# Performance work log

Hardware: AMD Instinct MI355X
Metric: run time of the kernel (lower is better)

Reference implementation:

```python
import jax, jax.numpy as jnp
import numpy as np

EPS = 1e-08


def _similarity_transform(S1, S2):
    """Batched Procrustes: S1, S2 are [B, 3, N]. Returns aligned S1_hat [B, 3, N]."""
    mu1 = jnp.mean(S1, axis=-1, keepdims=True)          # [B,3,1]
    mu2 = jnp.mean(S2, axis=-1, keepdims=True)
    X1 = S1 - mu1
    X2 = S2 - mu2
    var1 = jnp.sum(X1 * X1, axis=(1, 2))                # [B]
    # cross-covariance K = X1 @ X2^T + eps (eps added to every entry, as in torch ref)
    K = jnp.einsum('bin,bjn->bij', X1, X2) + EPS        # [B,3,3]
    U, s, Vh = jnp.linalg.svd(K, full_matrices=False)
    V = jnp.swapaxes(Vh, -1, -2)
    # det(U @ V^T) = det(U @ Vh); sign has zero gradient, same as torch
    sign = jax.lax.stop_gradient(jnp.sign(jnp.linalg.det(jnp.matmul(U, Vh))))  # [B]
    ones = jnp.ones_like(sign)
    d = jnp.stack([ones, ones, sign], axis=-1)          # diag of Z, [B,3]
    # R = V @ Z @ U^T
    R = jnp.einsum('bik,bk,bjk->bij', V, d, U)          # [B,3,3]
    scale = jnp.einsum('bij,bji->b', R, K) / var1       # trace(R@K)/var1, [B]
    t = mu2 - scale[:, None, None] * jnp.matmul(R, mu1)  # [B,3,1]
    S1_hat = scale[:, None, None] * jnp.matmul(R, S1) + t
    return S1_hat


def setup_inputs() -> dict:
    key = jax.random.key(0)
    k1, k2 = jax.random.split(key)
    B, N = 1024, 6890
    pred = jax.random.normal(k1, (B, N, 3), dtype=jnp.float32)
    gt = jax.random.normal(k2, (B, N, 3), dtype=jnp.float32)
    return {"pred": pred, "gt": gt}


def reference(pred, gt):
    # inputs are [B, N, 3] -> torch code transposes to [B, 3, N] and back
    S1 = jnp.swapaxes(pred, 1, 2)
    S2 = jnp.swapaxes(gt, 1, 2)
    S1_hat = jnp.swapaxes(_similarity_transform(S1, S2), 1, 2)  # [B,N,3]
    # loss_type == 'l1', reduction='none'
    return jnp.abs(S1_hat - gt)
```

## Files before the change

kernel.cpp:

```cpp
#include <hip/hip_runtime.h>
#include <math.h>

#define NPTS 6890
#define BATCH 1024
#define FLOATS_PER_BATCH (NPTS * 3)
#define NGROUPS 1722
#define CHUNKS 4
#define GPC 431
#define HALF_GROUPS 861

__device__ __forceinline__ void accum(float* acc, float p0, float p1, float p2,
                                      float g0, float g1, float g2) {
  acc[0] += p0;  acc[1] += p1;  acc[2] += p2;
  acc[3] += g0;  acc[4] += g1;  acc[5] += g2;
  acc[6] += p0 * p0 + p1 * p1 + p2 * p2;
  acc[7]  += p0 * g0;  acc[8]  += p0 * g1;  acc[9]  += p0 * g2;
  acc[10] += p1 * g0;  acc[11] += p1 * g1;  acc[12] += p1 * g2;
  acc[13] += p2 * g0;  acc[14] += p2 * g1;  acc[15] += p2 * g2;
}

__device__ __forceinline__ void accum_grp(float* acc, const float4 a0,
                                          const float4 a1, const float4 a2,
                                          const float4 c0, const float4 c1,
                                          const float4 c2) {
  accum(acc, a0.x, a0.y, a0.z, c0.x, c0.y, c0.z);
  accum(acc, a0.w, a1.x, a1.y, c0.w, c1.x, c1.y);
  accum(acc, a1.z, a1.w, a2.x, c1.z, c1.w, c2.x);
  accum(acc, a2.y, a2.z, a2.w, c2.y, c2.z, c2.w);
}

__global__ __launch_bounds__(256) void reduce_kernel(
    const float* __restrict__ pred, const float* __restrict__ gt,
    float* __restrict__ partials) {
  const int b = blockIdx.y;
  const int c = blockIdx.x;
  const size_t ofs0 = (size_t)b * FLOATS_PER_BATCH;
  const int skip = (b & 1) ? 2 : 0;
  const size_t ofs = ofs0 + (size_t)skip * 3;
  const float4* __restrict__ p4 = (const float4*)(pred + ofs);
  const float4* __restrict__ g4 = (const float4*)(gt + ofs);

  const int start = c * GPC;
  const int end = (c == CHUNKS - 1) ? NGROUPS : (start + GPC);

  float acc[16];
#pragma unroll
  for (int i = 0; i < 16; ++i) acc[i] = 0.f;

  const int g0 = start + (int)threadIdx.x;
  const int g1 = g0 + 256;
  const bool has1 = (g1 < end);

  const float4 a0 = p4[3 * g0], a1 = p4[3 * g0 + 1], a2 = p4[3 * g0 + 2];
  const float4 c0 = g4[3 * g0], c1 = g4[3 * g0 + 1], c2 = g4[3 * g0 + 2];
  float4 b0, b1, b2, d0, d1, d2;
  if (has1) {
    b0 = p4[3 * g1]; b1 = p4[3 * g1 + 1]; b2 = p4[3 * g1 + 2];
    d0 = g4[3 * g1]; d1 = g4[3 * g1 + 1]; d2 = g4[3 * g1 + 2];
  }
  accum_grp(acc, a0, a1, a2, c0, c1, c2);
  if (has1) accum_grp(acc, b0, b1, b2, d0, d1, d2);

  if (c == 0 && threadIdx.x < 2) {
    const int n = skip ? (int)threadIdx.x : (NPTS - 2 + (int)threadIdx.x);
    const float* pp = pred + ofs0 + 3 * n;
    const float* gg = gt + ofs0 + 3 * n;
    accum(acc, pp[0], pp[1], pp[2], gg[0], gg[1], gg[2]);
  }

#pragma unroll
  for (int i = 0; i < 16; ++i) {
#pragma unroll
    for (int off = 32; off > 0; off >>= 1)
      acc[i] += __shfl_down(acc[i], off, 64);
  }

  __shared__ float red[4][16];
  const int wave = threadIdx.x >> 6;
  const int lane = threadIdx.x & 63;
  if (lane == 0) {
#pragma unroll
    for (int i = 0; i < 16; ++i) red[wave][i] = acc[i];
  }
  __syncthreads();
  if (threadIdx.x < 16) {
    const int i = threadIdx.x;
    partials[(b * CHUNKS + c) * 16 + i] =
        red[0][i] + red[1][i] + red[2][i] + red[3][i];
  }
}

__global__ void solve_kernel(const float* __restrict__ partials,
                             float* __restrict__ params) {
  const int b = blockIdx.x * blockDim.x + threadIdx.x;
  if (b >= BATCH) return;

  float s[16];
#pragma unroll
  for (int i = 0; i < 16; ++i) {
    s[i] = partials[(b * CHUNKS + 0) * 16 + i] +
           partials[(b * CHUNKS + 1) * 16 + i] +
           partials[(b * CHUNKS + 2) * 16 + i] +
           partials[(b * CHUNKS + 3) * 16 + i];
  }
  const double Ninv = 1.0 / (double)NPTS;

  double sp[3] = {s[0], s[1], s[2]};
  double sg[3] = {s[3], s[4], s[5]};
  double mu1[3], mu2[3];
#pragma unroll
  for (int i = 0; i < 3; ++i) { mu1[i] = sp[i] * Ninv; mu2[i] = sg[i] * Ninv; }
  const double var1 =
      (double)s[6] - (sp[0] * sp[0] + sp[1] * sp[1] + sp[2] * sp[2]) * Ninv;

  double K[3][3];
#pragma unroll
  for (int i = 0; i < 3; ++i)
#pragma unroll
    for (int j = 0; j < 3; ++j)
      K[i][j] = (double)s[7 + 3 * i + j] - sp[i] * sg[j] * Ninv + 1e-8;

  double A[3][3];
#pragma unroll
  for (int i = 0; i < 3; ++i)
#pragma unroll
    for (int j = 0; j < 3; ++j)
      A[i][j] = K[0][i] * K[0][j] + K[1][i] * K[1][j] + K[2][i] * K[2][j];

  double V[3][3] = {{1, 0, 0}, {0, 1, 0}, {0, 0, 1}};
  for (int sweep = 0; sweep < 10; ++sweep) {
    const double off = A[0][1] * A[0][1] + A[0][2] * A[0][2] + A[1][2] * A[1][2];
    const double nrm = A[0][0] + A[1][1] + A[2][2];
    if (off <= 1e-26 * nrm * nrm) break;
    for (int pq = 0; pq < 3; ++pq) {
      const int p = (pq == 2) ? 1 : 0;
      const int q = (pq == 0) ? 1 : 2;
      const double apq = A[p][q];
      if (apq == 0.0) continue;
      const double theta = (A[q][q] - A[p][p]) / (2.0 * apq);
      const double tt =
          ((theta >= 0.0) ? 1.0 : -1.0) / (fabs(theta) + sqrt(theta * theta + 1.0));
      const double cj = 1.0 / sqrt(tt * tt + 1.0);
      const double sn = tt * cj;
      const double app = A[p][p], aqq = A[q][q];
      A[p][p] = app - tt * apq;
      A[q][q] = aqq + tt * apq;
      A[p][q] = 0.0; A[q][p] = 0.0;
      const int r = 3 - p - q;
      const double arp = A[r][p], arq = A[r][q];
      A[r][p] = cj * arp - sn * arq; A[p][r] = A[r][p];
      A[r][q] = sn * arp + cj * arq; A[q][r] = A[r][q];
#pragma unroll
      for (int k = 0; k < 3; ++k) {
        const double vkp = V[k][p], vkq = V[k][q];
        V[k][p] = cj * vkp - sn * vkq;
        V[k][q] = sn * vkp + cj * vkq;
      }
    }
  }

  double w[3] = {A[0][0], A[1][1], A[2][2]};
  int i0 = 0, i1 = 1, i2 = 2, tmp;
  if (w[i0] < w[i1]) { tmp = i0; i0 = i1; i1 = tmp; }
  if (w[i0] < w[i2]) { tmp = i0; i0 = i2; i2 = tmp; }
  if (w[i1] < w[i2]) { tmp = i1; i1 = i2; i2 = tmp; }
  const double sv0 = sqrt(fmax(w[i0], 0.0));
  const double sv1 = sqrt(fmax(w[i1], 0.0));
  const double sv2 = sqrt(fmax(w[i2], 0.0));

  const double detK =
      K[0][0] * (K[1][1] * K[2][2] - K[1][2] * K[2][1]) -
      K[0][1] * (K[1][0] * K[2][2] - K[1][2] * K[2][0]) +
      K[0][2] * (K[1][0] * K[2][1] - K[1][1] * K[2][0]);
  const double sgn = (detK > 0.0) ? 1.0 : ((detK < 0.0) ? -1.0 : 0.0);

  const double floor0 = sv0 * 1e-12 + 1e-300;
  const double z0 = 1.0 / fmax(sv0, floor0);
  const double z1 = 1.0 / fmax(sv1, floor0);
  const double z2 = sgn / fmax(sv2, floor0);

  double W[3][3];
#pragma unroll
  for (int a = 0; a < 3; ++a)
#pragma unroll
    for (int cc = 0; cc < 3; ++cc)
      W[a][cc] = V[a][i0] * V[cc][i0] * z0 + V[a][i1] * V[cc][i1] * z1 +
                 V[a][i2] * V[cc][i2] * z2;

  double R[3][3];
#pragma unroll
  for (int a = 0; a < 3; ++a)
#pragma unroll
    for (int cc = 0; cc < 3; ++cc)
      R[a][cc] = W[a][0] * K[cc][0] + W[a][1] * K[cc][1] + W[a][2] * K[cc][2];

  const double trace = sv0 + sv1 + sgn * sv2;
  const double scale = trace / var1;

  float* pr = params + b * 12;
#pragma unroll
  for (int a = 0; a < 3; ++a) {
#pragma unroll
    for (int cc = 0; cc < 3; ++cc) pr[3 * a + cc] = (float)(scale * R[a][cc]);
    pr[9 + a] = (float)(mu2[a] - scale * (R[a][0] * mu1[0] + R[a][1] * mu1[1] +
                                          R[a][2] * mu1[2]));
  }
}

__device__ __forceinline__ void xform(const float* m, float p0, float p1,
                                      float p2, float g0, float g1, float g2,
                                      float& o0, float& o1, float& o2) {
  o0 = fabsf(m[0] * p0 + m[1] * p1 + m[2] * p2 + m[9] - g0);
  o1 = fabsf(m[3] * p0 + m[4] * p1 + m[5] * p2 + m[10] - g1);
  o2 = fabsf(m[6] * p0 + m[7] * p1 + m[8] * p2 + m[11] - g2);
}

__device__ __forceinline__ void xform_grp(const float* m, const float4 a0,
                                          const float4 a1, const float4 a2,
                                          const float4 c0, const float4 c1,
                                          const float4 c2, float4& r0,
                                          float4& r1, float4& r2) {
  xform(m, a0.x, a0.y, a0.z, c0.x, c0.y, c0.z, r0.x, r0.y, r0.z);
  xform(m, a0.w, a1.x, a1.y, c0.w, c1.x, c1.y, r0.w, r1.x, r1.y);
  xform(m, a1.z, a1.w, a2.x, c1.z, c1.w, c2.x, r1.z, r1.w, r2.x);
  xform(m, a2.y, a2.z, a2.w, c2.y, c2.z, c2.w, r2.y, r2.z, r2.w);
}

__global__ __launch_bounds__(256) void apply_kernel(
    const float* __restrict__ pred, const float* __restrict__ gt,
    const float* __restrict__ params, float* __restrict__ out) {
  const int b = blockIdx.y;
  float m[12];
#pragma unroll
  for (int i = 0; i < 12; ++i) m[i] = params[b * 12 + i];

  const size_t ofs0 = (size_t)b * FLOATS_PER_BATCH;
  const int skip = (b & 1) ? 2 : 0;
  const size_t ofs = ofs0 + (size_t)skip * 3;
  const int idx = blockIdx.x * 256 + threadIdx.x;

  if (idx < HALF_GROUPS) {
    const int g0 = idx, g1 = idx + HALF_GROUPS;
    const float4* __restrict__ p4 = (const float4*)(pred + ofs);
    const float4* __restrict__ g4 = (const float4*)(gt + ofs);
    float4* __restrict__ o4 = (float4*)(out + ofs);
    const float4 a0 = p4[3 * g0], a1 = p4[3 * g0 + 1], a2 = p4[3 * g0 + 2];
    const float4 c0 = g4[3 * g0], c1 = g4[3 * g0 + 1], c2 = g4[3 * g0 + 2];
    const float4 b0 = p4[3 * g1], b1 = p4[3 * g1 + 1], b2 = p4[3 * g1 + 2];
    const float4 d0 = g4[3 * g1], d1 = g4[3 * g1 + 1], d2 = g4[3 * g1 + 2];
    float4 r0, r1, r2, q0, q1, q2;
    xform_grp(m, a0, a1, a2, c0, c1, c2, r0, r1, r2);
    xform_grp(m, b0, b1, b2, d0, d1, d2, q0, q1, q2);
    o4[3 * g0] = r0; o4[3 * g0 + 1] = r1; o4[3 * g0 + 2] = r2;
    o4[3 * g1] = q0; o4[3 * g1 + 1] = q1; o4[3 * g1 + 2] = q2;
  }

  if (blockIdx.x == 0 && threadIdx.x < 2) {
    const int n = skip ? (int)threadIdx.x : (NPTS - 2 + (int)threadIdx.x);
    const float* pp = pred + ofs0 + 3 * n;
    const float* gg = gt + ofs0 + 3 * n;
    float* oo = out + ofs0 + 3 * n;
    xform(m, pp[0], pp[1], pp[2], gg[0], gg[1], gg[2], oo[0], oo[1], oo[2]);
  }
}

extern "C" void kernel_launch(void* const* d_in, const int* in_sizes, int n_in,
                              void* d_out, int out_size, void* d_ws, size_t ws_size,
                              hipStream_t stream) {
  const float* pred = (const float*)d_in[0];
  const float* gt   = (const float*)d_in[1];
  float* out = (float*)d_out;
  float* partials = (float*)d_ws;
  float* params   = partials + BATCH * CHUNKS * 16;

  hipLaunchKernelGGL(reduce_kernel, dim3(CHUNKS, BATCH), dim3(256), 0, stream,
                     pred, gt, partials);
  hipLaunchKernelGGL(solve_kernel, dim3(16), dim3(64), 0, stream,
                     partials, params);
  hipLaunchKernelGGL(apply_kernel, dim3(4, BATCH), dim3(256), 0, stream,
                     pred, gt, params, out);
}
```

Baseline: 246.6 us.

## Stage float4 loads through LDS for coalesced access with register prefetch

Replaces the strided per-thread float4 loads (each thread reading 3 consecutive float4s) with fully coalesced loads that are transposed through shared memory, in both the reduce and apply kernels. Stores in the apply kernel are also staged through LDS so global writes are coalesced. Each block now covers half a batch over 4 iterations, with the next iteration's loads prefetched into registers while the current one is computed, and the chunk count drops from 4 to 2. This adds LDS traffic and extra barriers per iteration, and halves the number of blocks.

```diff
diff --git a/kernel.cpp b/kernel.cpp
--- a/kernel.cpp
+++ b/kernel.cpp
@@ -3,11 +3,12 @@
 
 #define NPTS 6890
 #define BATCH 1024
-#define FLOATS_PER_BATCH (NPTS * 3)
-#define NGROUPS 1722
-#define CHUNKS 4
-#define GPC 431
-#define HALF_GROUPS 861
+#define FPB (NPTS * 3)
+#define FQ 5166
+#define CHUNKS 2
+#define CFQ 2583
+#define SLOTS 768
+#define CITERS 4
 
 __device__ __forceinline__ void accum(float* acc, float p0, float p1, float p2,
                                       float g0, float g1, float g2) {
@@ -29,40 +30,65 @@
   accum(acc, a2.y, a2.z, a2.w, c2.y, c2.z, c2.w);
 }
 
+__device__ __forceinline__ void load_iter(const float4* __restrict__ p4,
+                                          const float4* __restrict__ g4,
+                                          int cstart, int limit, int it, int t,
+                                          float4* pk, float4* gk) {
+#pragma unroll
+  for (int k = 0; k < 3; ++k) {
+    const int f = cstart + it * SLOTS + k * 256 + t;
+    if (f < limit) {
+      pk[k] = p4[f];
+      gk[k] = g4[f];
+    } else {
+      pk[k] = make_float4(0.f, 0.f, 0.f, 0.f);
+      gk[k] = make_float4(0.f, 0.f, 0.f, 0.f);
+    }
+  }
+}
+
 __global__ __launch_bounds__(256) void reduce_kernel(
     const float* __restrict__ pred, const float* __restrict__ gt,
     float* __restrict__ partials) {
   const int b = blockIdx.y;
   const int c = blockIdx.x;
-  const size_t ofs0 = (size_t)b * FLOATS_PER_BATCH;
+  const int t = threadIdx.x;
+  const size_t ofs0 = (size_t)b * FPB;
   const int skip = (b & 1) ? 2 : 0;
   const size_t ofs = ofs0 + (size_t)skip * 3;
   const float4* __restrict__ p4 = (const float4*)(pred + ofs);
   const float4* __restrict__ g4 = (const float4*)(gt + ofs);
 
-  const int start = c * GPC;
-  const int end = (c == CHUNKS - 1) ? NGROUPS : (start + GPC);
+  const int cstart = c * CFQ;
+  const int limit = cstart + CFQ;
+
+  __shared__ float4 bufP[SLOTS];
+  __shared__ float4 bufG[SLOTS];
 
   float acc[16];
 #pragma unroll
   for (int i = 0; i < 16; ++i) acc[i] = 0.f;
 
-  const int g0 = start + (int)threadIdx.x;
-  const int g1 = g0 + 256;
-  const bool has1 = (g1 < end);
-
-  const float4 a0 = p4[3 * g0], a1 = p4[3 * g0 + 1], a2 = p4[3 * g0 + 2];
-  const float4 c0 = g4[3 * g0], c1 = g4[3 * g0 + 1], c2 = g4[3 * g0 + 2];
-  float4 b0, b1, b2, d0, d1, d2;
-  if (has1) {
-    b0 = p4[3 * g1]; b1 = p4[3 * g1 + 1]; b2 = p4[3 * g1 + 2];
-    d0 = g4[3 * g1]; d1 = g4[3 * g1 + 1]; d2 = g4[3 * g1 + 2];
-  }
-  accum_grp(acc, a0, a1, a2, c0, c1, c2);
-  if (has1) accum_grp(acc, b0, b1, b2, d0, d1, d2);
-
-  if (c == 0 && threadIdx.x < 2) {
-    const int n = skip ? (int)threadIdx.x : (NPTS - 2 + (int)threadIdx.x);
+  float4 pk[3], gk[3];
+  load_iter(p4, g4, cstart, limit, 0, t, pk, gk);
+
+  for (int it = 0; it < CITERS; ++it) {
+    __syncthreads();
+#pragma unroll
+    for (int k = 0; k < 3; ++k) {
+      bufP[k * 256 + t] = pk[k];
+      bufG[k * 256 + t] = gk[k];
+    }
+    __syncthreads();
+    if (it + 1 < CITERS)
+      load_iter(p4, g4, cstart, limit, it + 1, t, pk, gk);
+    const float4 x0 = bufP[3 * t], x1 = bufP[3 * t + 1], x2 = bufP[3 * t + 2];
+    const float4 y0 = bufG[3 * t], y1 = bufG[3 * t + 1], y2 = bufG[3 * t + 2];
+    accum_grp(acc, x0, x1, x2, y0, y1, y2);
+  }
+
+  if (c == 0 && t < 2) {
+    const int n = skip ? t : (NPTS - 2 + t);
     const float* pp = pred + ofs0 + 3 * n;
     const float* gg = gt + ofs0 + 3 * n;
     accum(acc, pp[0], pp[1], pp[2], gg[0], gg[1], gg[2]);
@@ -76,18 +102,16 @@
   }
 
   __shared__ float red[4][16];
-  const int wave = threadIdx.x >> 6;
-  const int lane = threadIdx.x & 63;
+  const int wave = t >> 6;
+  const int lane = t & 63;
   if (lane == 0) {
 #pragma unroll
     for (int i = 0; i < 16; ++i) red[wave][i] = acc[i];
   }
   __syncthreads();
-  if (threadIdx.x < 16) {
-    const int i = threadIdx.x;
-    partials[(b * CHUNKS + c) * 16 + i] =
-        red[0][i] + red[1][i] + red[2][i] + red[3][i];
-  }
+  if (t < 16)
+    partials[(b * CHUNKS + c) * 16 + t] =
+        red[0][t] + red[1][t] + red[2][t] + red[3][t];
 }
 
 __global__ void solve_kernel(const float* __restrict__ partials,
@@ -97,14 +121,11 @@
 
   float s[16];
 #pragma unroll
-  for (int i = 0; i < 16; ++i) {
+  for (int i = 0; i < 16; ++i)
     s[i] = partials[(b * CHUNKS + 0) * 16 + i] +
-           partials[(b * CHUNKS + 1) * 16 + i] +
-           partials[(b * CHUNKS + 2) * 16 + i] +
-           partials[(b * CHUNKS + 3) * 16 + i];
-  }
+           partials[(b * CHUNKS + 1) * 16 + i];
+
   const double Ninv = 1.0 / (double)NPTS;
-
   double sp[3] = {s[0], s[1], s[2]};
   double sg[3] = {s[3], s[4], s[5]};
   double mu1[3], mu2[3];
@@ -230,33 +251,54 @@
     const float* __restrict__ pred, const float* __restrict__ gt,
     const float* __restrict__ params, float* __restrict__ out) {
   const int b = blockIdx.y;
+  const int c = blockIdx.x;
+  const int t = threadIdx.x;
   float m[12];
 #pragma unroll
   for (int i = 0; i < 12; ++i) m[i] = params[b * 12 + i];
 
-  const size_t ofs0 = (size_t)b * FLOATS_PER_BATCH;
+  const size_t ofs0 = (size_t)b * FPB;
   const int skip = (b & 1) ? 2 : 0;
   const size_t ofs = ofs0 + (size_t)skip * 3;
-  const int idx = blockIdx.x * 256 + threadIdx.x;
-
-  if (idx < HALF_GROUPS) {
-    const int g0 = idx, g1 = idx + HALF_GROUPS;
-    const float4* __restrict__ p4 = (const float4*)(pred + ofs);
-    const float4* __restrict__ g4 = (const float4*)(gt + ofs);
-    float4* __restrict__ o4 = (float4*)(out + ofs);
-    const float4 a0 = p4[3 * g0], a1 = p4[3 * g0 + 1], a2 = p4[3 * g0 + 2];
-    const float4 c0 = g4[3 * g0], c1 = g4[3 * g0 + 1], c2 = g4[3 * g0 + 2];
-    const float4 b0 = p4[3 * g1], b1 = p4[3 * g1 + 1], b2 = p4[3 * g1 + 2];
-    const float4 d0 = g4[3 * g1], d1 = g4[3 * g1 + 1], d2 = g4[3 * g1 + 2];
-    float4 r0, r1, r2, q0, q1, q2;
-    xform_grp(m, a0, a1, a2, c0, c1, c2, r0, r1, r2);
-    xform_grp(m, b0, b1, b2, d0, d1, d2, q0, q1, q2);
-    o4[3 * g0] = r0; o4[3 * g0 + 1] = r1; o4[3 * g0 + 2] = r2;
-    o4[3 * g1] = q0; o4[3 * g1 + 1] = q1; o4[3 * g1 + 2] = q2;
-  }
-
-  if (blockIdx.x == 0 && threadIdx.x < 2) {
-    const int n = skip ? (int)threadIdx.x : (NPTS - 2 + (int)threadIdx.x);
+  const float4* __restrict__ p4 = (const float4*)(pred + ofs);
+  const float4* __restrict__ g4 = (const float4*)(gt + ofs);
+  float4* __restrict__ o4 = (float4*)(out + ofs);
+
+  const int cstart = c * CFQ;
+  const int limit = cstart + CFQ;
+
+  __shared__ float4 bufP[SLOTS];
+  __shared__ float4 bufG[SLOTS];
+
+  float4 pk[3], gk[3];
+  load_iter(p4, g4, cstart, limit, 0, t, pk, gk);
+
+  for (int it = 0; it < CITERS; ++it) {
+    __syncthreads();
+#pragma unroll
+    for (int k = 0; k < 3; ++k) {
+      bufP[k * 256 + t] = pk[k];
+      bufG[k * 256 + t] = gk[k];
+    }
+    __syncthreads();
+    if (it + 1 < CITERS)
+      load_iter(p4, g4, cstart, limit, it + 1, t, pk, gk);
+
+    const float4 x0 = bufP[3 * t], x1 = bufP[3 * t + 1], x2 = bufP[3 * t + 2];
+    const float4 y0 = bufG[3 * t], y1 = bufG[3 * t + 1], y2 = bufG[3 * t + 2];
+    float4 r0, r1, r2;
+    xform_grp(m, x0, x1, x2, y0, y1, y2, r0, r1, r2);
+    bufG[3 * t] = r0; bufG[3 * t + 1] = r1; bufG[3 * t + 2] = r2;
+    __syncthreads();
+#pragma unroll
+    for (int k = 0; k < 3; ++k) {
+      const int f = cstart + it * SLOTS + k * 256 + t;
+      if (f < limit) o4[f] = bufG[k * 256 + t];
+    }
+  }
+
+  if (c == 0 && t < 2) {
+    const int n = skip ? t : (NPTS - 2 + t);
     const float* pp = pred + ofs0 + 3 * n;
     const float* gg = gt + ofs0 + 3 * n;
     float* oo = out + ofs0 + 3 * n;
@@ -277,6 +319,6 @@
                      pred, gt, partials);
   hipLaunchKernelGGL(solve_kernel, dim3(16), dim3(64), 0, stream,
                      partials, params);
-  hipLaunchKernelGGL(apply_kernel, dim3(4, BATCH), dim3(256), 0, stream,
+  hipLaunchKernelGGL(apply_kernel, dim3(CHUNKS, BATCH), dim3(256), 0, stream,
                      pred, gt, params, out);
 }
```

Result: no change. 248.2 us (+0.6%).

## Stage reduce-kernel loads through LDS with async global_load_lds double buffering

Applied to the files above, without the earlier changes.

Rewrites the per-batch reduction kernel to use 2 chunks per batch instead of 4. Each block streams its float4 data into double-buffered LDS with global_load_lds DMA, uses manual waitcnt values to overlap loads with accumulation, and handles a small tail with direct loads. The aim is more bytes in flight per block and fewer blocks and partials, so HBM bandwidth is better used during the reduction. The hand-coded waitcnt encodings and fixed slot arithmetic are fragile, and halving the grid may reduce parallelism.

```diff
diff --git a/kernel.cpp b/kernel.cpp
--- a/kernel.cpp
+++ b/kernel.cpp
@@ -1,13 +1,38 @@
 #include <hip/hip_runtime.h>
 #include <math.h>
+#include <stdint.h>
 
 #define NPTS 6890
 #define BATCH 1024
-#define FLOATS_PER_BATCH (NPTS * 3)
-#define NGROUPS 1722
-#define CHUNKS 4
-#define GPC 431
+#define FPB (NPTS * 3)
+#define FQ 5166
+#define CHUNKS 2
+#define CFQ 2583
+#define SLOTS 768
+#define DITERS 3
 #define HALF_GROUPS 861
+
+#define WAIT_VM6 0x0F76
+#define WAIT_VM0 0x0F70
+#define WAIT_LGKM0 0xC07F
+
+__device__ __forceinline__ void dma16(const float4* g, float4* l) {
+  __builtin_amdgcn_global_load_lds(
+      (const __attribute__((address_space(1))) void*)g,
+      (__attribute__((address_space(3))) void*)l, 16, 0, 0);
+}
+
+__device__ __forceinline__ void stage(const float4* __restrict__ p4,
+                                      const float4* __restrict__ g4, int fbase,
+                                      float4* bp, float4* bg, int t) {
+  const int w = t >> 6, lane = t & 63;
+#pragma unroll
+  for (int j = 0; j < 3; ++j) {
+    const int s = w * 192 + j * 64 + lane;
+    dma16(p4 + fbase + s, bp + s);
+    dma16(g4 + fbase + s, bg + s);
+  }
+}
 
 __device__ __forceinline__ void accum(float* acc, float p0, float p1, float p2,
                                       float g0, float g1, float g2) {
@@ -34,35 +59,61 @@
     float* __restrict__ partials) {
   const int b = blockIdx.y;
   const int c = blockIdx.x;
-  const size_t ofs0 = (size_t)b * FLOATS_PER_BATCH;
+  const int t = threadIdx.x;
+  const size_t ofs0 = (size_t)b * FPB;
   const int skip = (b & 1) ? 2 : 0;
   const size_t ofs = ofs0 + (size_t)skip * 3;
   const float4* __restrict__ p4 = (const float4*)(pred + ofs);
   const float4* __restrict__ g4 = (const float4*)(gt + ofs);
-
-  const int start = c * GPC;
-  const int end = (c == CHUNKS - 1) ? NGROUPS : (start + GPC);
+  const int cstart = c * CFQ;
+
+  __shared__ float4 bufP[2][SLOTS];
+  __shared__ float4 bufG[2][SLOTS];
 
   float acc[16];
 #pragma unroll
   for (int i = 0; i < 16; ++i) acc[i] = 0.f;
 
-  const int g0 = start + (int)threadIdx.x;
-  const int g1 = g0 + 256;
-  const bool has1 = (g1 < end);
-
-  const float4 a0 = p4[3 * g0], a1 = p4[3 * g0 + 1], a2 = p4[3 * g0 + 2];
-  const float4 c0 = g4[3 * g0], c1 = g4[3 * g0 + 1], c2 = g4[3 * g0 + 2];
-  float4 b0, b1, b2, d0, d1, d2;
-  if (has1) {
-    b0 = p4[3 * g1]; b1 = p4[3 * g1 + 1]; b2 = p4[3 * g1 + 2];
-    d0 = g4[3 * g1]; d1 = g4[3 * g1 + 1]; d2 = g4[3 * g1 + 2];
-  }
-  accum_grp(acc, a0, a1, a2, c0, c1, c2);
-  if (has1) accum_grp(acc, b0, b1, b2, d0, d1, d2);
-
-  if (c == 0 && threadIdx.x < 2) {
-    const int n = skip ? (int)threadIdx.x : (NPTS - 2 + (int)threadIdx.x);
+  stage(p4, g4, cstart + 0 * SLOTS, bufP[0], bufG[0], t);
+  stage(p4, g4, cstart + 1 * SLOTS, bufP[1], bufG[1], t);
+
+  const int w = t >> 6, lane = t & 63;
+  const int bs = w * 192 + 3 * lane;
+
+  {
+    __builtin_amdgcn_s_waitcnt(WAIT_VM6);
+    __asm__ __volatile__("" ::: "memory");
+    const float4 x0 = bufP[0][bs], x1 = bufP[0][bs + 1], x2 = bufP[0][bs + 2];
+    const float4 y0 = bufG[0][bs], y1 = bufG[0][bs + 1], y2 = bufG[0][bs + 2];
+    __builtin_amdgcn_s_waitcnt(WAIT_LGKM0);
+    __asm__ __volatile__("" ::: "memory");
+    stage(p4, g4, cstart + 2 * SLOTS, bufP[0], bufG[0], t);
+    accum_grp(acc, x0, x1, x2, y0, y1, y2);
+  }
+  {
+    __builtin_amdgcn_s_waitcnt(WAIT_VM6);
+    __asm__ __volatile__("" ::: "memory");
+    const float4 x0 = bufP[1][bs], x1 = bufP[1][bs + 1], x2 = bufP[1][bs + 2];
+    const float4 y0 = bufG[1][bs], y1 = bufG[1][bs + 1], y2 = bufG[1][bs + 2];
+    accum_grp(acc, x0, x1, x2, y0, y1, y2);
+  }
+  {
+    __builtin_amdgcn_s_waitcnt(WAIT_VM0);
+    __asm__ __volatile__("" ::: "memory");
+    const float4 x0 = bufP[0][bs], x1 = bufP[0][bs + 1], x2 = bufP[0][bs + 2];
+    const float4 y0 = bufG[0][bs], y1 = bufG[0][bs + 1], y2 = bufG[0][bs + 2];
+    accum_grp(acc, x0, x1, x2, y0, y1, y2);
+  }
+
+  if (t < 93) {
+    const int f = cstart + DITERS * SLOTS + 3 * t;
+    const float4 x0 = p4[f], x1 = p4[f + 1], x2 = p4[f + 2];
+    const float4 y0 = g4[f], y1 = g4[f + 1], y2 = g4[f + 2];
+    accum_grp(acc, x0, x1, x2, y0, y1, y2);
+  }
+
+  if (c == 0 && t < 2) {
+    const int n = skip ? t : (NPTS - 2 + t);
     const float* pp = pred + ofs0 + 3 * n;
     const float* gg = gt + ofs0 + 3 * n;
     accum(acc, pp[0], pp[1], pp[2], gg[0], gg[1], gg[2]);
@@ -76,18 +127,14 @@
   }
 
   __shared__ float red[4][16];
-  const int wave = threadIdx.x >> 6;
-  const int lane = threadIdx.x & 63;
   if (lane == 0) {
 #pragma unroll
-    for (int i = 0; i < 16; ++i) red[wave][i] = acc[i];
+    for (int i = 0; i < 16; ++i) red[w][i] = acc[i];
   }
   __syncthreads();
-  if (threadIdx.x < 16) {
-    const int i = threadIdx.x;
-    partials[(b * CHUNKS + c) * 16 + i] =
-        red[0][i] + red[1][i] + red[2][i] + red[3][i];
-  }
+  if (t < 16)
+    partials[(b * CHUNKS + c) * 16 + t] =
+        red[0][t] + red[1][t] + red[2][t] + red[3][t];
 }
 
 __global__ void solve_kernel(const float* __restrict__ partials,
@@ -97,14 +144,11 @@
 
   float s[16];
 #pragma unroll
-  for (int i = 0; i < 16; ++i) {
+  for (int i = 0; i < 16; ++i)
     s[i] = partials[(b * CHUNKS + 0) * 16 + i] +
-           partials[(b * CHUNKS + 1) * 16 + i] +
-           partials[(b * CHUNKS + 2) * 16 + i] +
-           partials[(b * CHUNKS + 3) * 16 + i];
-  }
+           partials[(b * CHUNKS + 1) * 16 + i];
+
   const double Ninv = 1.0 / (double)NPTS;
-
   double sp[3] = {s[0], s[1], s[2]};
   double sg[3] = {s[3], s[4], s[5]};
   double mu1[3], mu2[3];
@@ -234,7 +278,7 @@
 #pragma unroll
   for (int i = 0; i < 12; ++i) m[i] = params[b * 12 + i];
 
-  const size_t ofs0 = (size_t)b * FLOATS_PER_BATCH;
+  const size_t ofs0 = (size_t)b * FPB;
   const int skip = (b & 1) ? 2 : 0;
   const size_t ofs = ofs0 + (size_t)skip * 3;
   const int idx = blockIdx.x * 256 + threadIdx.x;
```

Measured after the change: 249.4 us. About the same (+1.1%).
